# Optimization experiments

Measured on AMD Instinct MI355X. Metric: run time of the kernel, lower is better.

The kernel has to match this reference:

```python
import jax, jax.numpy as jnp
import numpy as np

B, L, K = 256, 128, 6
FA, FB, D = 39, 10, 128
R, T = 3, 2
NEG = -9e8


def _gru(x, h, wih, whh, bih, bhh):
    # torch.nn.GRUCell semantics
    gi = x @ wih.T + bih
    gh = h @ whh.T + bhh
    ir, iz, inn = jnp.split(gi, 3, axis=-1)
    hr, hz, hn = jnp.split(gh, 3, axis=-1)
    r = jax.nn.sigmoid(ir + hr)
    z = jax.nn.sigmoid(iz + hz)
    n = jnp.tanh(inn + r * hn)
    return (1.0 - z) * n + z * h


def _forward(atom_list, bond_list, atom_mask, atom_fc_w, atom_fc_b, nbr_fc_w, nbr_fc_b,
             align_w, align_b, attend_w, attend_b, gru_wih, gru_whh, gru_bih, gru_bhh,
             mol_align_w, mol_align_b, mol_attend_w, mol_attend_b,
             mol_gru_wih, mol_gru_whh, mol_gru_bih, mol_gru_bhh, out_w, out_b,
             atom_degree_list, bond_degree_list):
    lrelu = jax.nn.leaky_relu  # slope 0.01, matches torch default
    bidx = jnp.arange(atom_list.shape[0])[:, None, None]
    gather = lambda f, idx: f[bidx, idx]  # [B,L,F] gathered by [B,L,K] -> [B,L,K,F]

    atom_feature = lrelu(atom_list @ atom_fc_w + atom_fc_b)  # [B,L,D]
    nbr = jnp.concatenate([gather(atom_list, atom_degree_list),
                           gather(bond_list, bond_degree_list)], axis=-1)
    nbr = lrelu(nbr @ nbr_fc_w + nbr_fc_b)  # [B,L,K,D]

    pad = atom_list.shape[1] - 1  # mol_length-1 is padding sentinel
    attend_mask = (atom_degree_list != pad).astype(atom_feature.dtype)[..., None]
    softmax_mask = jnp.where(atom_degree_list == pad, NEG, 0.0).astype(atom_feature.dtype)[..., None]

    def attn(cur, nbr_feat, aw, ab, tw, tb):
        exp = jnp.broadcast_to(cur[:, :, None, :], nbr_feat.shape)
        score = lrelu(jnp.concatenate([exp, nbr_feat], axis=-1) @ aw + ab) + softmax_mask
        w = jax.nn.softmax(score, axis=-2) * attend_mask  # softmax over neighbors
        return jax.nn.elu(jnp.sum(w * (nbr_feat @ tw + tb), axis=-2))

    h = atom_feature
    ctx = attn(atom_feature, nbr, align_w[0], align_b[0], attend_w[0], attend_b[0])
    h = _gru(ctx, h, gru_wih[0], gru_whh[0], gru_bih[0], gru_bhh[0])
    act = jax.nn.relu(h)
    for d in range(1, R):
        nbr_f = gather(act, atom_degree_list)
        ctx = attn(act, nbr_f, align_w[d], align_b[d], attend_w[d], attend_b[d])
        h = _gru(ctx, h, gru_wih[d], gru_whh[d], gru_bih[d], gru_bhh[d])
        act = jax.nn.relu(h)

    am = atom_mask[..., None]  # [B,L,1]
    mol_feature = jnp.sum(act * am, axis=-2)  # [B,D]
    act_mol = jax.nn.relu(mol_feature)
    mol_smask = jnp.where(am == 0, NEG, 0.0).astype(atom_feature.dtype)
    for _ in range(T):
        exp = jnp.broadcast_to(act_mol[:, None, :], act.shape)
        score = lrelu(jnp.concatenate([exp, act], axis=-1) @ mol_align_w + mol_align_b) + mol_smask
        w = jax.nn.softmax(score, axis=-2) * am  # softmax over atoms
        ctx = jax.nn.elu(jnp.sum(w * (act @ mol_attend_w + mol_attend_b), axis=-2))
        mol_feature = _gru(ctx, mol_feature, mol_gru_wih, mol_gru_whh, mol_gru_bih, mol_gru_bhh)
        act_mol = jax.nn.relu(mol_feature)
    mol_prediction = mol_feature @ out_w + out_b  # [B,1]
    return h, mol_prediction


def setup_inputs():
    key = jax.random.key(0)
    ks = jax.random.split(key, 30)
    f = lambda i, s: jax.random.normal(ks[i], s, dtype=jnp.float32) * 0.1
    return {
        'atom_list': jax.random.normal(ks[0], (B, L, FA), dtype=jnp.float32),
        'bond_list': jax.random.normal(ks[1], (B, L, FB), dtype=jnp.float32),
        'atom_mask': jnp.ones((B, L), jnp.float32),
        'atom_fc_w': f(2, (FA, D)), 'atom_fc_b': f(3, (D,)),
        'nbr_fc_w': f(4, (FA + FB, D)), 'nbr_fc_b': f(5, (D,)),
        'align_w': f(6, (R, 2 * D, 1)), 'align_b': f(7, (R, 1)),
        'attend_w': f(8, (R, D, D)), 'attend_b': f(9, (R, D)),
        'gru_wih': f(10, (R, 3 * D, D)), 'gru_whh': f(11, (R, 3 * D, D)),
        'gru_bih': f(12, (R, 3 * D)), 'gru_bhh': f(13, (R, 3 * D)),
        'mol_align_w': f(14, (2 * D, 1)), 'mol_align_b': f(15, (1,)),
        'mol_attend_w': f(16, (D, D)), 'mol_attend_b': f(17, (D,)),
        'mol_gru_wih': f(18, (3 * D, D)), 'mol_gru_whh': f(19, (3 * D, D)),
        'mol_gru_bih': f(20, (3 * D,)), 'mol_gru_bhh': f(21, (3 * D,)),
        'out_w': f(22, (D, 1)), 'out_b': f(23, (1,)),
        'atom_degree_list': jax.random.randint(ks[24], (B, L, K), 0, L),
        'bond_degree_list': jax.random.randint(ks[25], (B, L, K), 0, L),
    }


def reference(atom_list, bond_list, atom_mask, atom_fc_w, atom_fc_b, nbr_fc_w, nbr_fc_b,
              align_w, align_b, attend_w, attend_b, gru_wih, gru_whh, gru_bih, gru_bhh,
              mol_align_w, mol_align_b, mol_attend_w, mol_attend_b,
              mol_gru_wih, mol_gru_whh, mol_gru_bih, mol_gru_bhh, out_w, out_b,
              atom_degree_list, bond_degree_list):
    return _forward(atom_list, bond_list, atom_mask, atom_fc_w, atom_fc_b, nbr_fc_w, nbr_fc_b,
                    align_w, align_b, attend_w, attend_b, gru_wih, gru_whh, gru_bih, gru_bhh,
                    mol_align_w, mol_align_b, mol_attend_w, mol_attend_b,
                    mol_gru_wih, mol_gru_whh, mol_gru_bih, mol_gru_bhh, out_w, out_b,
                    atom_degree_list, bond_degree_list)
```

## Files before the change

kernel.cpp:

```cpp
#include <hip/hip_runtime.h>
#include <cstddef>


#define B_ 256
#define L_ 128
#define K_ 6
#define FA_ 39
#define FB_ 10
#define D_ 128
#define PAD_ 127
#define NEGC (-9.0e8f)
#define NA 32
#define NPAIR (NA * K_)

typedef unsigned short u16;
typedef unsigned int u32;
using s8 = __attribute__((ext_vector_type(8))) short;
using f4 = __attribute__((ext_vector_type(4))) float;

#define WIH_H 0
#define WIH_L 49152
#define WHH_H 98304
#define WHH_L 147456
#define TW_H  196608
#define TW_L  212992
#define RND_BLK2 229376
#define NB16 (3 * RND_BLK2)
#define NMOLF (2 * 128 * 384)

__device__ __forceinline__ float lrelu(float x) { return x > 0.f ? x : 0.01f * x; }
__device__ __forceinline__ float eluf(float x)  { return x > 0.f ? x : expm1f(x); }
__device__ __forceinline__ float sigm(float x)  { return 1.f / (1.f + expf(-x)); }
__device__ __forceinline__ float b2f(u16 u) {
  union { u32 i; float f; } v; v.i = ((u32)u) << 16; return v.f;
}
__device__ __forceinline__ short f2b(float f) {
  union { float f; u32 i; } v; v.f = f;
  u32 x = v.i;
  return (short)(u16)((x + 0x7FFFu + ((x >> 16) & 1u)) >> 16);
}

__global__ __launch_bounds__(256) void k_tr(
    const float* __restrict__ gwih, const float* __restrict__ gwhh,
    const float* __restrict__ attw,
    const float* __restrict__ mwih, const float* __restrict__ mwhh,
    short* __restrict__ wB, float* __restrict__ molT) {
  int idx = blockIdx.x * 256 + threadIdx.x;
  if (idx < NB16) {
    int r = idx / RND_BLK2, o = idx % RND_BLK2;
    float v; int lo;
    int e, kind;
    if (o < 98304)      { kind = 0; lo = o / 49152; e = o % 49152; }
    else if (o < 196608){ kind = 1; int o2 = o - 98304; lo = o2 / 49152; e = o2 % 49152; }
    else                { kind = 2; int o2 = o - 196608; lo = o2 / 16384; e = o2 % 16384; }
    int gt = e >> 11, rem = e & 2047;
    int kc = rem >> 9, rem2 = rem & 511;
    int lane = rem2 >> 3, j = rem2 & 7;
    int col = lane & 15, quad = lane >> 4;
    int g = gt * 16 + col;
    int k = kc * 32 + quad * 8 + j;
    if (kind == 0)      v = gwih[(size_t)r * 49152 + g * 128 + k];
// ... 86 lines not shown
    const short* __restrict__ APg, float* __restrict__ Q0g)
{
  int tid = threadIdx.x;
  __shared__ float WbS[10 * 128];
  __shared__ float nbS[128], ahS[128];
  for (int i = tid; i < 10 * 128; i += 256)
    WbS[i] = nbr_w[(FA_ + i / 128) * D_ + (i % 128)];
  if (tid < 128) { nbS[tid] = nbr_b[tid]; ahS[tid] = aw0[D_ + tid]; }
  __syncthreads();

  int p = blockIdx.x * 64 + (tid >> 2);
  int seg = tid & 3;
  int aidx = adeg[p], bidx = bdeg[p];
  int bb = p / (L_ * K_);
  const short* rowA = APg + ((size_t)bb * L_ + aidx) * D_;
  const float* brow = bond_list + ((size_t)bb * L_ + bidx) * FB_;
  float bnd[10];
#pragma unroll
  for (int m = 0; m < 10; m++) bnd[m] = brow[m];
  float s = 0.f;
  int j0 = seg * 32;
#pragma unroll 4
  for (int j = j0; j < j0 + 32; j++) {
    float v = b2f((u16)rowA[j]) + nbS[j];
#pragma unroll
    for (int m = 0; m < 10; m++) v += bnd[m] * WbS[m * 128 + j];
    s += lrelu(v) * ahS[j];
  }
  s += __shfl_xor(s, 1, 64);
  s += __shfl_xor(s, 2, 64);
  if (seg == 0) Q0g[p] = s;
}

template <int FIRST>
__global__ __launch_bounds__(512, 4) void k_round(
    const u16* __restrict__ hin,
    u16* __restrict__ hout,
    const float* __restrict__ bond_list,
    const int* __restrict__ adeg, const int* __restrict__ bdeg,
    const float* __restrict__ nbr_w, const float* __restrict__ nbr_b,
    const short* __restrict__ APg,
    const float* __restrict__ ab,
    const float* __restrict__ awN,
    const float* __restrict__ tb,
    const short* __restrict__ wR,
    const float* __restrict__ bih, const float* __restrict__ bhh,
    const float* __restrict__ Pr, const float* __restrict__ Qr,
    float* __restrict__ Pw, float* __restrict__ Qw)
{
  int tid  = threadIdx.x;
  int lane = tid & 63;
  int wv   = tid >> 6;
  int quad = lane >> 4;
  int col  = lane & 15;
  int aT   = tid >> 4;
  int dg   = (tid & 15) * 8;
  int tile = (blockIdx.x & 7) * 128 + (blockIdx.x >> 3);
  int a0   = tile * NA;
  int bb   = a0 >> 7;

  const short* wihH = wR + WIH_H;
  const short* wihL = wR + WIH_L;
  const short* whhH = wR + WHH_H;
  const short* whhL = wR + WHH_L;
  const short* twH  = wR + TW_H;
  const short* twL  = wR + TW_L;

  __shared__ short hrowH[NA][136];
  __shared__ __align__(16) char arena[17408];
  __shared__ float awNS[256];
  __shared__ float partials[512];
  __shared__ float pS[NA], qS[NPAIR], wkS[NPAIR], wsS[NA];
  __shared__ int aidxS[NPAIR];
  __shared__ int bidxS[FIRST ? NPAIR : 1];
  __shared__ float bwS[FIRST ? 1920 : 1];

  short* ybarH = (short*)arena;
  short* ybarL = (short*)(arena + 8704);
  float* hnrel = (float*)arena;

  if (tid < NPAIR) {
    int av = adeg[a0 * K_ + tid];
    aidxS[tid] = av;
    if (FIRST) { bidxS[tid] = bdeg[a0 * K_ + tid]; qS[tid] = Qr[a0 * K_ + tid]; }
    else       qS[tid] = Qr[bb * L_ + av];
  } else if (tid < NPAIR + NA) {
    pS[tid - NPAIR] = Pr[a0 + (tid - NPAIR)];
  }
  if (tid < 256) awNS[tid] = awN[tid];
  __syncthreads();

  if (FIRST) {
    for (int i = tid; i < NPAIR * 10; i += 512) {
      int p = i / 10, m = i % 10;
      bwS[p * 10 + m] = bond_list[((size_t)bb * L_ + bidxS[p]) * FB_ + m];
    }
  }
  *(s8*)&hrowH[aT][dg] = *(const s8*)&hin[(size_t)(a0 + aT) * D_ + dg];

  if (tid < NA) {
    int a = tid;
    float abv = ab[0];
    float sc[K_];
    float m = -3.0e38f;
#pragma unroll
    for (int k = 0; k < K_; k++) {
      float s = lrelu(pS[a] + qS[a * K_ + k] + abv);
      if (aidxS[a * K_ + k] == PAD_) s += NEGC;
      sc[k] = s; m = fmaxf(m, s);
    }
    float es = 0.f;
#pragma unroll
    for (int k = 0; k < K_; k++) { sc[k] = expf(sc[k] - m); es += sc[k]; }
    float ws = 0.f;
#pragma unroll
    for (int k = 0; k < K_; k++) {
      float w = (aidxS[a * K_ + k] == PAD_) ? 0.f : sc[k] / es;
      wkS[a * K_ + k] = w; ws += w;
    }
    wsS[a] = ws;
  }
  __syncthreads();

  {
    float yb[8];
#pragma unroll
    for (int j = 0; j < 8; j++) yb[j] = 0.f;
    if (FIRST) {
#pragma unroll
      for (int h = 0; h < 2; h++) {
        float Wr[10][4];
#pragma unroll
        for (int m = 0; m < 10; m++) {
          float4 w = *(const float4*)&nbr_w[(FA_ + m) * D_ + dg + h * 4];
          Wr[m][0] = w.x; Wr[m][1] = w.y; Wr[m][2] = w.z; Wr[m][3] = w.w;
        }
        float4 nb4 = *(const float4*)&nbr_b[dg + h * 4];
        float nb[4] = {nb4.x, nb4.y, nb4.z, nb4.w};
#pragma unroll
        for (int k = 0; k < K_; k++) {
          int p = aT * K_ + k;
          ushort4 ap4 = *(const ushort4*)&APg[((size_t)bb * L_ + aidxS[p]) * D_ + dg + h * 4];
          float nf[4] = { b2f(ap4.x) + nb[0], b2f(ap4.y) + nb[1],
                          b2f(ap4.z) + nb[2], b2f(ap4.w) + nb[3] };
#pragma unroll
          for (int m = 0; m < 10; m++) {
            float bv = bwS[p * 10 + m];
#pragma unroll
            for (int j = 0; j < 4; j++) nf[j] += bv * Wr[m][j];
          }
          float w = wkS[p];
#pragma unroll
          for (int j = 0; j < 4; j++) yb[h * 4 + j] += w * lrelu(nf[j]);
        }
      }
    } else {
#pragma unroll
      for (int k = 0; k < K_; k++) {
        int p = aT * K_ + k;
        float w = wkS[p];
        s8 hv8 = *(const s8*)&hin[((size_t)bb * L_ + aidxS[p]) * D_ + dg];
#pragma unroll
        for (int j = 0; j < 8; j++) yb[j] += w * fmaxf(b2f((u16)hv8[j]), 0.f);
      }
    }
    s8 yh8, yl8;
#pragma unroll
    for (int j = 0; j < 8; j++) {
      short hi = f2b(yb[j]);
      yh8[j] = hi;
      yl8[j] = f2b(yb[j] - b2f((u16)hi));
    }
    *(s8*)&ybarH[aT * 136 + dg] = yh8;
    *(s8*)&ybarL[aT * 136 + dg] = yl8;
  }
  __syncthreads();

  {
    f4 c2[2] = {};
#pragma unroll
    for (int k0c = 0; k0c < 4; k0c++) {
      int fo = ((wv * 4 + k0c) * 64 + lane) * 8;
      s8 bwh = *(const s8*)&twH[fo];
      s8 bwl = *(const s8*)&twL[fo];
#pragma unroll
      for (int at = 0; at < 2; at++) {
        s8 ayh = *(const s8*)&ybarH[(at * 16 + col) * 136 + k0c * 32 + quad * 8];
        s8 ayl = *(const s8*)&ybarL[(at * 16 + col) * 136 + k0c * 32 + quad * 8];
        c2[at] = __builtin_amdgcn_mfma_f32_16x16x32_bf16(ayh, bwh, c2[at], 0, 0, 0);
        c2[at] = __builtin_amdgcn_mfma_f32_16x16x32_bf16(ayl, bwh, c2[at], 0, 0, 0);
        c2[at] = __builtin_amdgcn_mfma_f32_16x16x32_bf16(ayh, bwl, c2[at], 0, 0, 0);
      }
    }
    __syncthreads();
    int g = wv * 16 + col;
    float tbv = tb[g];
#pragma unroll
    for (int at = 0; at < 2; at++) {
#pragma unroll
      for (int r = 0; r < 4; r++) {
        int a = at * 16 + quad * 4 + r;
        float c = eluf(c2[at][r] + wsS[a] * tbv);
        short chs = f2b(c);
        ybarH[a * 136 + g] = chs;
        ybarL[a * 136 + g] = f2b(c - b2f((u16)chs));
      }
    }
  }
  __syncthreads();

  {
    const short* ctxH = ybarH;
    const short* ctxL = ybarL;
    f4 gi[2][3] = {}, gh[2][3] = {};
#pragma unroll
    for (int k0c = 0; k0c < 4; k0c++) {
      s8 ach[2], acl[2], ahh[2];
#pragma unroll
      for (int at = 0; at < 2; at++) {
        ach[at] = *(const s8*)&ctxH[(at * 16 + col) * 136 + k0c * 32 + quad * 8];
        acl[at] = *(const s8*)&ctxL[(at * 16 + col) * 136 + k0c * 32 + quad * 8];
        ahh[at] = *(const s8*)&hrowH[at * 16 + col][k0c * 32 + quad * 8];
      }
#pragma unroll
      for (int kd = 0; kd < 3; kd++) {
        int gt = wv + kd * 8;
        int fo = ((gt * 4 + k0c) * 64 + lane) * 8;
        s8 bi_h = *(const s8*)&wihH[fo];
        s8 bi_l = *(const s8*)&wihL[fo];
        s8 bh_h = *(const s8*)&whhH[fo];
        s8 bh_l = *(const s8*)&whhL[fo];
#pragma unroll
        for (int at = 0; at < 2; at++) {
          gi[at][kd] = __builtin_amdgcn_mfma_f32_16x16x32_bf16(ach[at], bi_h, gi[at][kd], 0, 0, 0);
          gi[at][kd] = __builtin_amdgcn_mfma_f32_16x16x32_bf16(acl[at], bi_h, gi[at][kd], 0, 0, 0);
          gi[at][kd] = __builtin_amdgcn_mfma_f32_16x16x32_bf16(ach[at], bi_l, gi[at][kd], 0, 0, 0);
          gh[at][kd] = __builtin_amdgcn_mfma_f32_16x16x32_bf16(ahh[at], bh_h, gh[at][kd], 0, 0, 0);
          gh[at][kd] = __builtin_amdgcn_mfma_f32_16x16x32_bf16(ahh[at], bh_l, gh[at][kd], 0, 0, 0);
        }
      }
    }
    __syncthreads();

    {
      int ic = wv * 16 + col;
      float bi0 = bih[ic], bi1 = bih[D_ + ic], bi2 = bih[2 * D_ + ic];
      float bh0 = bhh[ic], bh1 = bhh[D_ + ic], bh2 = bhh[2 * D_ + ic];
#pragma unroll
      for (int at = 0; at < 2; at++) {
#pragma unroll
        for (int r = 0; r < 4; r++) {
          int a = at * 16 + quad * 4 + r;
          float rr = sigm(gi[at][0][r] + bi0 + gh[at][0][r] + bh0);
          float zz = sigm(gi[at][1][r] + bi1 + gh[at][1][r] + bh1);
          float nn = tanhf(gi[at][2][r] + bi2 + rr * (gh[at][2][r] + bh2));
          float hv = b2f((u16)hrowH[a][ic]);
          float hn = (1.f - zz) * nn + zz * hv;
          hrowH[a][ic] = f2b(hn);
          if (Pw) hnrel[a * 132 + ic] = fmaxf(hn, 0.f);
        }
      }
    }
  }
  __syncthreads();

  *(s8*)&hout[(size_t)(a0 + aT) * D_ + dg] = *(const s8*)&hrowH[aT][dg];

  if (Pw) {
    {
      int a = tid >> 4, dt = (tid >> 3) & 1, seg = tid & 7;
      float s = 0.f;
#pragma unroll
      for (int j = 0; j < 16; j++)
        s += hnrel[a * 132 + seg * 16 + j] * awNS[dt * 128 + seg * 16 + j];
      partials[tid] = s;
    }
    __syncthreads();
    if (tid < 64) {
      int a = tid >> 1, dt = tid & 1;
      float s = 0.f;
#pragma unroll
      for (int seg = 0; seg < 8; seg++) s += partials[a * 16 + dt * 8 + seg];
      if (dt) Qw[a0 + a] = s; else Pw[a0 + a] = s;
    }
  }
}

__device__ __forceinline__ float blk_sum128(float v, int tid, float* redS) {
  if (tid < 128) {
#pragma unroll
    for (int s = 1; s < 64; s <<= 1) v += __shfl_xor(v, s, 64);
    if ((tid & 63) == 0) redS[tid >> 6] = v;
  }
  __syncthreads();
  float r = redS[0] + redS[1];
  __syncthreads();
  return r;
}
__device__ __forceinline__ float blk_max128(float v, int tid, float* redS) {
  if (tid < 128) {
#pragma unroll
    for (int s = 1; s < 64; s <<= 1) v = fmaxf(v, __shfl_xor(v, s, 64));
    if ((tid & 63) == 0) redS[tid >> 6] = v;
  }
  __syncthreads();
  float r = fmaxf(redS[0], redS[1]);
  __syncthreads();
  return r;
}

__global__ __launch_bounds__(512) void k_mol(
    const u16* __restrict__ hfin,
    float* __restrict__ hcopy,
    const float* __restrict__ amask,
    const float* __restrict__ maw, const float* __restrict__ mab,
    const float* __restrict__ mtw, const float* __restrict__ mtb,
    const float* __restrict__ wih_t, const float* __restrict__ whh_t,
    const float* __restrict__ bih, const float* __restrict__ bhh,
    const float* __restrict__ ow, const float* __restrict__ ob,
    float* __restrict__ pred)
{
  int b = blockIdx.x;
  int tid = threadIdx.x;
  int t128 = tid & 127;
  int qf = tid >> 7;
  __shared__ float actS[L_][D_ + 1];
  __shared__ float redS[2];
  __shared__ float par4[4][132];
  __shared__ float pg[3][6][132];
  __shared__ float wgt[128], ybv[132], ctx[132], mfS[132], amol[132];
  __shared__ float msk[128], mawh[128], scf[128];

  if (qf == 0) { msk[t128] = amask[b * L_ + t128]; mawh[t128] = maw[D_ + t128]; }
  for (int i = 0; i < 32; i++) {
    int l = qf * 32 + i;
    float hv = b2f(hfin[(size_t)(b * L_ + l) * D_ + t128]);
    hcopy[(size_t)(b * L_ + l) * D_ + t128] = hv;
    actS[l][t128] = fmaxf(hv, 0.f);
  }
  __syncthreads();

  {
    float s = 0.f;
    for (int i = 0; i < 32; i++) { int l = qf * 32 + i; s += actS[l][t128] * msk[l]; }
    par4[qf][t128] = s;
  }
  __syncthreads();
  if (qf == 0) {
    float mf = par4[0][t128] + par4[1][t128] + par4[2][t128] + par4[3][t128];
    mfS[t128] = mf; amol[t128] = fmaxf(mf, 0.f);
  }
  __syncthreads();

  float mabv = mab[0];

  for (int t = 0; t < 2; t++) {
    float s0 = blk_sum128((tid < 128) ? amol[tid] * maw[tid] : 0.f, tid, redS);

    {
      float s = 0.f;
      for (int i = 0; i < 32; i++) { int j = qf * 32 + i; s += actS[t128][j] * mawh[j]; }
      par4[qf][t128] = s;
    }
    __syncthreads();
    if (qf == 0) {
      float sc = lrelu(s0 + mabv + par4[0][t128] + par4[1][t128] + par4[2][t128] + par4[3][t128]);
      if (msk[t128] == 0.f) sc += NEGC;
      scf[t128] = sc;
    }
    __syncthreads();

    float scv = scf[t128];
    float mx = blk_max128((tid < 128) ? scv : -3.0e38f, tid, redS);
    float e = expf(scv - mx);
    float es = blk_sum128((tid < 128) ? e : 0.f, tid, redS);
    float w = (e / es) * msk[t128];
    if (qf == 0) wgt[t128] = w;
    float wsum = blk_sum128((tid < 128) ? w : 0.f, tid, redS);

    {
      float s = 0.f;
      for (int i = 0; i < 32; i++) { int l = qf * 32 + i; s += wgt[l] * actS[l][t128]; }
      par4[qf][t128] = s;
    }
    __syncthreads();
    if (qf == 0) ybv[t128] = par4[0][t128] + par4[1][t128] + par4[2][t128] + par4[3][t128];
    __syncthreads();

    {
      float s = 0.f;
#pragma unroll 2
      for (int i = 0; i < 32; i++) { int j = qf * 32 + i; s += ybv[j] * mtw[j * D_ + t128]; }
      par4[qf][t128] = s;
    }
    __syncthreads();
    if (qf == 0)
      ctx[t128] = eluf(par4[0][t128] + par4[1][t128] + par4[2][t128] + par4[3][t128]
                       + wsum * mtb[t128]);
    __syncthreads();

    {
      float gi0 = 0, gi1 = 0, gi2 = 0, gh0 = 0, gh1 = 0, gh2 = 0;
#pragma unroll 2
      for (int i = 0; i < 32; i++) {
        int j = qf * 32 + i;
        const float* wi = wih_t + (size_t)j * 384;
        const float* wh = whh_t + (size_t)j * 384;
        float xc = ctx[j], xh = mfS[j];
        gi0 += xc * wi[t128]; gi1 += xc * wi[128 + t128]; gi2 += xc * wi[256 + t128];
        gh0 += xh * wh[t128]; gh1 += xh * wh[128 + t128]; gh2 += xh * wh[256 + t128];
      }
      if (qf > 0) {
        pg[qf - 1][0][t128] = gi0; pg[qf - 1][1][t128] = gi1; pg[qf - 1][2][t128] = gi2;
        pg[qf - 1][3][t128] = gh0; pg[qf - 1][4][t128] = gh1; pg[qf - 1][5][t128] = gh2;
      }
      __syncthreads();
      if (qf == 0) {
        gi0 += pg[0][0][t128] + pg[1][0][t128] + pg[2][0][t128] + bih[t128];
        gi1 += pg[0][1][t128] + pg[1][1][t128] + pg[2][1][t128] + bih[128 + t128];
        gi2 += pg[0][2][t128] + pg[1][2][t128] + pg[2][2][t128] + bih[256 + t128];
        gh0 += pg[0][3][t128] + pg[1][3][t128] + pg[2][3][t128] + bhh[t128];
        gh1 += pg[0][4][t128] + pg[1][4][t128] + pg[2][4][t128] + bhh[128 + t128];
        gh2 += pg[0][5][t128] + pg[1][5][t128] + pg[2][5][t128] + bhh[256 + t128];
        float r = sigm(gi0 + gh0);
        float z = sigm(gi1 + gh1);
        float n = tanhf(gi2 + r * gh2);
        float hn = (1.f - z) * n + z * mfS[t128];
        mfS[t128] = hn;
        amol[t128] = fmaxf(hn, 0.f);
      }
      __syncthreads();
    }
  }

  float fin = blk_sum128((tid < 128) ? mfS[tid] * ow[tid] : 0.f, tid, redS);
  if (tid == 0) pred[b] = fin + ob[0];
}

extern "C" void kernel_launch(void* const* d_in, const int* in_sizes, int n_in,
                              void* d_out, int out_size, void* d_ws, size_t ws_size,
                              hipStream_t stream) {
  const float* atom_list    = (const float*)d_in[0];
  const float* bond_list    = (const float*)d_in[1];
  const float* atom_mask    = (const float*)d_in[2];
  const float* atom_fc_w    = (const float*)d_in[3];
  const float* atom_fc_b    = (const float*)d_in[4];
  const float* nbr_fc_w     = (const float*)d_in[5];
  const float* nbr_fc_b     = (const float*)d_in[6];
  const float* align_w      = (const float*)d_in[7];
  const float* align_b      = (const float*)d_in[8];
  const float* attend_w     = (const float*)d_in[9];
  const float* attend_b     = (const float*)d_in[10];
  const float* gru_wih      = (const float*)d_in[11];
  const float* gru_whh      = (const float*)d_in[12];
  const float* gru_bih      = (const float*)d_in[13];
  const float* gru_bhh      = (const float*)d_in[14];
  const float* mol_align_w  = (const float*)d_in[15];
  const float* mol_align_b  = (const float*)d_in[16];
  const float* mol_attend_w = (const float*)d_in[17];
  const float* mol_attend_b = (const float*)d_in[18];
  const float* mol_gru_wih  = (const float*)d_in[19];
  const float* mol_gru_whh  = (const float*)d_in[20];
  const float* mol_gru_bih  = (const float*)d_in[21];
  const float* mol_gru_bhh  = (const float*)d_in[22];
  const float* out_w        = (const float*)d_in[23];
  const float* out_b        = (const float*)d_in[24];
  const int*   adeg         = (const int*)d_in[25];
  const int*   bdeg         = (const int*)d_in[26];

  const size_t NH = (size_t)B_ * L_ * D_;
  u16*   hA   = (u16*)d_ws;
  u16*   hB   = hA + NH;
  short* wB   = (short*)(hB + NH);
  float* molT = (float*)(wB + NB16);
  float* PgA  = molT + NMOLF;
  float* QgA  = PgA + B_ * L_;
  float* PgB  = QgA + B_ * L_;
  float* QgB  = PgB + B_ * L_;
  short* APg  = (short*)(QgB + B_ * L_);
  float* Q0g  = (float*)(APg + NH);
  float* hOut = (float*)d_out;
  float* pred = hOut + NH;

  k_tr<<<dim3((NB16 + NMOLF + 255) / 256), dim3(256), 0, stream>>>(
      gru_wih, gru_whh, attend_w, mol_gru_wih, mol_gru_whh, wB, molT);

  k_pre<<<dim3(B_ * L_ / 16), dim3(128), 0, stream>>>(
      atom_list, atom_fc_w, atom_fc_b, nbr_fc_w, align_w, hA, APg, PgA);
  k_q0<<<dim3(B_ * L_ * K_ / 64), dim3(256), 0, stream>>>(
      bond_list, nbr_fc_w, nbr_fc_b, align_w, adeg, bdeg, APg, Q0g);

  dim3 blk(512), grd(B_ * L_ / NA);

  k_round<1><<<grd, blk, 0, stream>>>(
      hA, hB, bond_list, adeg, bdeg, nbr_fc_w, nbr_fc_b, APg,
      align_b, align_w + 2 * D_, attend_b,
      wB + 0 * (size_t)RND_BLK2, gru_bih, gru_bhh,
      PgA, Q0g, PgB, QgB);
  k_round<0><<<grd, blk, 0, stream>>>(
      hB, hA, bond_list, adeg, bdeg, nbr_fc_w, nbr_fc_b, APg,
      align_b + 1, align_w + 4 * D_, attend_b + D_,
      wB + 1 * (size_t)RND_BLK2, gru_bih + 3 * D_, gru_bhh + 3 * D_,
      PgB, QgB, PgA, QgA);
  k_round<0><<<grd, blk, 0, stream>>>(
      hA, hB, bond_list, adeg, bdeg, nbr_fc_w, nbr_fc_b, APg,
      align_b + 2, align_w + 4 * D_, attend_b + 2 * D_,
      wB + 2 * (size_t)RND_BLK2, gru_bih + 6 * D_, gru_bhh + 6 * D_,
      PgA, QgA, (float*)nullptr, (float*)nullptr);

  k_mol<<<dim3(B_), dim3(512), 0, stream>>>(
      hB, hOut, atom_mask, mol_align_w, mol_align_b, mol_attend_w, mol_attend_b,
      molT, molT + 128 * 384,
      mol_gru_bih, mol_gru_bhh, out_w, out_b, pred);
}
```

Baseline: 328.2 us.

## Fuse three message-passing rounds and molecule readout into one per-molecule kernel

Measured after the change: 808.5 us. +146.4%, slower.

```diff
diff --git a/kernel.cpp b/kernel.cpp
--- a/kernel.cpp
+++ b/kernel.cpp
@@ -10,8 +10,6 @@
 #define D_ 128
 #define PAD_ 127
 #define NEGC (-9.0e8f)
-#define NA 32
-#define NPAIR (NA * K_)
 
 typedef unsigned short u16;
 typedef unsigned int u32;
@@ -27,6 +25,20 @@
 #define RND_BLK2 229376
 #define NB16 (3 * RND_BLK2)
 #define NMOLF (2 * 128 * 384)
+
+#define OFF_HS     0
+#define OFF_ARENA  34816
+#define OFF_BWS    104448
+#define OFF_AIDX   135168
+#define OFF_WK     138240
+#define OFF_PA     141312
+#define OFF_QA     141824
+#define OFF_WS     142336
+#define OFF_AWN    142848
+#define OFF_PPART  143872
+#define OFF_QPART  147968
+#define OFF_MOLM   152064
+#define SMEM_BYTES 156176
 
 __device__ __forceinline__ float lrelu(float x) { return x > 0.f ? x : 0.01f * x; }
 __device__ __forceinline__ float eluf(float x)  { return x > 0.f ? x : expm1f(x); }
@@ -179,339 +191,359 @@
   if (seg == 0) Q0g[p] = s;
 }
 
-template <int FIRST>
-__global__ __launch_bounds__(512, 4) void k_round(
-    const u16* __restrict__ hin,
-    u16* __restrict__ hout,
+__device__ __forceinline__ float blk_sum128(float v, int tid, float* redS) {
+  if (tid < 128) {
+#pragma unroll
+    for (int s = 1; s < 64; s <<= 1) v += __shfl_xor(v, s, 64);
+    if ((tid & 63) == 0) redS[tid >> 6] = v;
+  }
+  __syncthreads();
+  float r = redS[0] + redS[1];
+  __syncthreads();
+  return r;
+}
+__device__ __forceinline__ float blk_max128(float v, int tid, float* redS) {
+  if (tid < 128) {
+#pragma unroll
+    for (int s = 1; s < 64; s <<= 1) v = fmaxf(v, __shfl_xor(v, s, 64));
+    if ((tid & 63) == 0) redS[tid >> 6] = v;
+  }
+  __syncthreads();
+  float r = fmaxf(redS[0], redS[1]);
+  __syncthreads();
+  return r;
+}
+
+__global__ __launch_bounds__(1024, 4) void k_mega(
+    const u16* __restrict__ hA,
     const float* __restrict__ bond_list,
     const int* __restrict__ adeg, const int* __restrict__ bdeg,
     const float* __restrict__ nbr_w, const float* __restrict__ nbr_b,
     const short* __restrict__ APg,
-    const float* __restrict__ ab,
-    const float* __restrict__ awN,
-    const float* __restrict__ tb,
-    const short* __restrict__ wR,
-    const float* __restrict__ bih, const float* __restrict__ bhh,
-    const float* __restrict__ Pr, const float* __restrict__ Qr,
-    float* __restrict__ Pw, float* __restrict__ Qw)
-{
-  int tid  = threadIdx.x;
-  int lane = tid & 63;
-  int wv   = tid >> 6;
-  int quad = lane >> 4;
-  int col  = lane & 15;
-  int aT   = tid >> 4;
-  int dg   = (tid & 15) * 8;
-  int tile = (blockIdx.x & 7) * 128 + (blockIdx.x >> 3);
-  int a0   = tile * NA;
-  int bb   = a0 >> 7;
-
-  const short* wihH = wR + WIH_H;
-  const short* wihL = wR + WIH_L;
-  const short* whhH = wR + WHH_H;
-  const short* whhL = wR + WHH_L;
-  const short* twH  = wR + TW_H;
-  const short* twL  = wR + TW_L;
-
-  __shared__ short hrowH[NA][136];
-  __shared__ __align__(16) char arena[17408];
-  __shared__ float awNS[256];
-  __shared__ float partials[512];
-  __shared__ float pS[NA], qS[NPAIR], wkS[NPAIR], wsS[NA];
-  __shared__ int aidxS[NPAIR];
-  __shared__ int bidxS[FIRST ? NPAIR : 1];
-  __shared__ float bwS[FIRST ? 1920 : 1];
-
-  short* ybarH = (short*)arena;
-  short* ybarL = (short*)(arena + 8704);
-  float* hnrel = (float*)arena;
-
-  if (tid < NPAIR) {
-    int av = adeg[a0 * K_ + tid];
-    aidxS[tid] = av;
-    if (FIRST) { bidxS[tid] = bdeg[a0 * K_ + tid]; qS[tid] = Qr[a0 * K_ + tid]; }
-    else       qS[tid] = Qr[bb * L_ + av];
-  } else if (tid < NPAIR + NA) {
-    pS[tid - NPAIR] = Pr[a0 + (tid - NPAIR)];
-  }
-  if (tid < 256) awNS[tid] = awN[tid];
-  __syncthreads();
-
-  if (FIRST) {
-    for (int i = tid; i < NPAIR * 10; i += 512) {
-      int p = i / 10, m = i % 10;
-      bwS[p * 10 + m] = bond_list[((size_t)bb * L_ + bidxS[p]) * FB_ + m];
-    }
-  }
-  *(s8*)&hrowH[aT][dg] = *(const s8*)&hin[(size_t)(a0 + aT) * D_ + dg];
-
-  if (tid < NA) {
-    int a = tid;
-    float abv = ab[0];
-    float sc[K_];
-    float m = -3.0e38f;
-#pragma unroll
-    for (int k = 0; k < K_; k++) {
-      float s = lrelu(pS[a] + qS[a * K_ + k] + abv);
-      if (aidxS[a * K_ + k] == PAD_) s += NEGC;
-      sc[k] = s; m = fmaxf(m, s);
-    }
-    float es = 0.f;
-#pragma unroll
-    for (int k = 0; k < K_; k++) { sc[k] = expf(sc[k] - m); es += sc[k]; }
-    float ws = 0.f;
-#pragma unroll
-    for (int k = 0; k < K_; k++) {
-      float w = (aidxS[a * K_ + k] == PAD_) ? 0.f : sc[k] / es;
-      wkS[a * K_ + k] = w; ws += w;
-    }
-    wsS[a] = ws;
-  }
-  __syncthreads();
-
-  {
-    float yb[8];
-#pragma unroll
-    for (int j = 0; j < 8; j++) yb[j] = 0.f;
-    if (FIRST) {
-#pragma unroll
-      for (int h = 0; h < 2; h++) {
-        float Wr[10][4];
-#pragma unroll
-        for (int m = 0; m < 10; m++) {
-          float4 w = *(const float4*)&nbr_w[(FA_ + m) * D_ + dg + h * 4];
-          Wr[m][0] = w.x; Wr[m][1] = w.y; Wr[m][2] = w.z; Wr[m][3] = w.w;
-        }
-        float4 nb4 = *(const float4*)&nbr_b[dg + h * 4];
-        float nb[4] = {nb4.x, nb4.y, nb4.z, nb4.w};
-#pragma unroll
-        for (int k = 0; k < K_; k++) {
-          int p = aT * K_ + k;
-          ushort4 ap4 = *(const ushort4*)&APg[((size_t)bb * L_ + aidxS[p]) * D_ + dg + h * 4];
-          float nf[4] = { b2f(ap4.x) + nb[0], b2f(ap4.y) + nb[1],
-                          b2f(ap4.z) + nb[2], b2f(ap4.w) + nb[3] };
-#pragma unroll
-          for (int m = 0; m < 10; m++) {
-            float bv = bwS[p * 10 + m];
-#pragma unroll
-            for (int j = 0; j < 4; j++) nf[j] += bv * Wr[m][j];
-          }
-          float w = wkS[p];
-#pragma unroll
-          for (int j = 0; j < 4; j++) yb[h * 4 + j] += w * lrelu(nf[j]);
-        }
-      }
-    } else {
-#pragma unroll
-      for (int k = 0; k < K_; k++) {
-        int p = aT * K_ + k;
-        float w = wkS[p];
-        s8 hv8 = *(const s8*)&hin[((size_t)bb * L_ + aidxS[p]) * D_ + dg];
-#pragma unroll
-        for (int j = 0; j < 8; j++) yb[j] += w * fmaxf(b2f((u16)hv8[j]), 0.f);
-      }
-    }
-    s8 yh8, yl8;
-#pragma unroll
-    for (int j = 0; j < 8; j++) {
-      short hi = f2b(yb[j]);
-      yh8[j] = hi;
-      yl8[j] = f2b(yb[j] - b2f((u16)hi));
-    }
-    *(s8*)&ybarH[aT * 136 + dg] = yh8;
-    *(s8*)&ybarL[aT * 136 + dg] = yl8;
-  }
-  __syncthreads();
-
-  {
-    f4 c2[2] = {};
-#pragma unroll
-    for (int k0c = 0; k0c < 4; k0c++) {
-      int fo = ((wv * 4 + k0c) * 64 + lane) * 8;
-      s8 bwh = *(const s8*)&twH[fo];
-      s8 bwl = *(const s8*)&twL[fo];
-#pragma unroll
-      for (int at = 0; at < 2; at++) {
-        s8 ayh = *(const s8*)&ybarH[(at * 16 + col) * 136 + k0c * 32 + quad * 8];
-        s8 ayl = *(const s8*)&ybarL[(at * 16 + col) * 136 + k0c * 32 + quad * 8];
-        c2[at] = __builtin_amdgcn_mfma_f32_16x16x32_bf16(ayh, bwh, c2[at], 0, 0, 0);
-        c2[at] = __builtin_amdgcn_mfma_f32_16x16x32_bf16(ayl, bwh, c2[at], 0, 0, 0);
-        c2[at] = __builtin_amdgcn_mfma_f32_16x16x32_bf16(ayh, bwl, c2[at], 0, 0, 0);
-      }
-    }
-    __syncthreads();
-    int g = wv * 16 + col;
-    float tbv = tb[g];
-#pragma unroll
-    for (int at = 0; at < 2; at++) {
-#pragma unroll
-      for (int r = 0; r < 4; r++) {
-        int a = at * 16 + quad * 4 + r;
-        float c = eluf(c2[at][r] + wsS[a] * tbv);
-        short chs = f2b(c);
-        ybarH[a * 136 + g] = chs;
-        ybarL[a * 136 + g] = f2b(c - b2f((u16)chs));
-      }
-    }
-  }
-  __syncthreads();
-
-  {
-    const short* ctxH = ybarH;
-    const short* ctxL = ybarL;
-    f4 gi[2][3] = {}, gh[2][3] = {};
-#pragma unroll
-    for (int k0c = 0; k0c < 4; k0c++) {
-      s8 ach[2], acl[2], ahh[2];
-#pragma unroll
-      for (int at = 0; at < 2; at++) {
-        ach[at] = *(const s8*)&ctxH[(at * 16 + col) * 136 + k0c * 32 + quad * 8];
-        acl[at] = *(const s8*)&ctxL[(at * 16 + col) * 136 + k0c * 32 + quad * 8];
-        ahh[at] = *(const s8*)&hrowH[at * 16 + col][k0c * 32 + quad * 8];
-      }
-#pragma unroll
-      for (int kd = 0; kd < 3; kd++) {
-        int gt = wv + kd * 8;
-        int fo = ((gt * 4 + k0c) * 64 + lane) * 8;
-        s8 bi_h = *(const s8*)&wihH[fo];
-        s8 bi_l = *(const s8*)&wihL[fo];
-        s8 bh_h = *(const s8*)&whhH[fo];
-        s8 bh_l = *(const s8*)&whhL[fo];
-#pragma unroll
-        for (int at = 0; at < 2; at++) {
-          gi[at][kd] = __builtin_amdgcn_mfma_f32_16x16x32_bf16(ach[at], bi_h, gi[at][kd], 0, 0, 0);
-          gi[at][kd] = __builtin_amdgcn_mfma_f32_16x16x32_bf16(acl[at], bi_h, gi[at][kd], 0, 0, 0);
-          gi[at][kd] = __builtin_amdgcn_mfma_f32_16x16x32_bf16(ach[at], bi_l, gi[at][kd], 0, 0, 0);
-          gh[at][kd] = __builtin_amdgcn_mfma_f32_16x16x32_bf16(ahh[at], bh_h, gh[at][kd], 0, 0, 0);
-          gh[at][kd] = __builtin_amdgcn_mfma_f32_16x16x32_bf16(ahh[at], bh_l, gh[at][kd], 0, 0, 0);
-        }
-      }
-    }
-    __syncthreads();
-
-    {
-      int ic = wv * 16 + col;
-      float bi0 = bih[ic], bi1 = bih[D_ + ic], bi2 = bih[2 * D_ + ic];
-      float bh0 = bhh[ic], bh1 = bhh[D_ + ic], bh2 = bhh[2 * D_ + ic];
-#pragma unroll
-      for (int at = 0; at < 2; at++) {
-#pragma unroll
-        for (int r = 0; r < 4; r++) {
-          int a = at * 16 + quad * 4 + r;
-          float rr = sigm(gi[at][0][r] + bi0 + gh[at][0][r] + bh0);
-          float zz = sigm(gi[at][1][r] + bi1 + gh[at][1][r] + bh1);
-          float nn = tanhf(gi[at][2][r] + bi2 + rr * (gh[at][2][r] + bh2));
-          float hv = b2f((u16)hrowH[a][ic]);
-          float hn = (1.f - zz) * nn + zz * hv;
-          hrowH[a][ic] = f2b(hn);
-          if (Pw) hnrel[a * 132 + ic] = fmaxf(hn, 0.f);
-        }
-      }
-    }
-  }
-  __syncthreads();
-
-  *(s8*)&hout[(size_t)(a0 + aT) * D_ + dg] = *(const s8*)&hrowH[aT][dg];
-
-  if (Pw) {
-    {
-      int a = tid >> 4, dt = (tid >> 3) & 1, seg = tid & 7;
-      float s = 0.f;
-#pragma unroll
-      for (int j = 0; j < 16; j++)
-        s += hnrel[a * 132 + seg * 16 + j] * awNS[dt * 128 + seg * 16 + j];
-      partials[tid] = s;
-    }
-    __syncthreads();
-    if (tid < 64) {
-      int a = tid >> 1, dt = tid & 1;
-      float s = 0.f;
-#pragma unroll
-      for (int seg = 0; seg < 8; seg++) s += partials[a * 16 + dt * 8 + seg];
-      if (dt) Qw[a0 + a] = s; else Pw[a0 + a] = s;
-    }
-  }
-}
-
-__device__ __forceinline__ float blk_sum128(float v, int tid, float* redS) {
-  if (tid < 128) {
-#pragma unroll
-    for (int s = 1; s < 64; s <<= 1) v += __shfl_xor(v, s, 64);
-    if ((tid & 63) == 0) redS[tid >> 6] = v;
-  }
-  __syncthreads();
-  float r = redS[0] + redS[1];
-  __syncthreads();
-  return r;
-}
-__device__ __forceinline__ float blk_max128(float v, int tid, float* redS) {
-  if (tid < 128) {
-#pragma unroll
-    for (int s = 1; s < 64; s <<= 1) v = fmaxf(v, __shfl_xor(v, s, 64));
-    if ((tid & 63) == 0) redS[tid >> 6] = v;
-  }
-  __syncthreads();
-  float r = fmaxf(redS[0], redS[1]);
-  __syncthreads();
-  return r;
-}
-
-__global__ __launch_bounds__(512) void k_mol(
-    const u16* __restrict__ hfin,
-    float* __restrict__ hcopy,
+    const float* __restrict__ align_b_all,
+    const float* __restrict__ align_w_all,
+    const float* __restrict__ attend_b_all,
+    const short* __restrict__ wB,
+    const float* __restrict__ bih_all, const float* __restrict__ bhh_all,
+    const float* __restrict__ PgA, const float* __restrict__ Q0g,
     const float* __restrict__ amask,
     const float* __restrict__ maw, const float* __restrict__ mab,
     const float* __restrict__ mtw, const float* __restrict__ mtb,
     const float* __restrict__ wih_t, const float* __restrict__ whh_t,
-    const float* __restrict__ bih, const float* __restrict__ bhh,
+    const float* __restrict__ mbih, const float* __restrict__ mbhh,
     const float* __restrict__ ow, const float* __restrict__ ob,
-    float* __restrict__ pred)
+    float* __restrict__ hcopy, float* __restrict__ pred)
 {
-  int b = blockIdx.x;
-  int tid = threadIdx.x;
+  __shared__ __align__(16) char smem[SMEM_BYTES];
+  short* hS    = (short*)(smem + OFF_HS);
+  char*  arena = smem + OFF_ARENA;
+  short* ybH   = (short*)arena;
+  short* ybL   = (short*)(arena + 34816);
+  float* actS  = (float*)arena;
+  float* bwS   = (float*)(smem + OFF_BWS);
+  float* pg    = bwS;
+  float* par8  = bwS + 5544;
+  int*   aidxS = (int*)(smem + OFF_AIDX);
+  float* wkS   = (float*)(smem + OFF_WK);
+  float* pAS   = (float*)(smem + OFF_PA);
+  float* qAS   = (float*)(smem + OFF_QA);
+  float* wsS   = (float*)(smem + OFF_WS);
+  float* awNS  = (float*)(smem + OFF_AWN);
+  float* pPart = (float*)(smem + OFF_PPART);
+  float* qPart = (float*)(smem + OFF_QPART);
+  float* molm  = (float*)(smem + OFF_MOLM);
+  float* wgt = molm, *ybv = molm + 128, *ctxv = molm + 256, *mfS = molm + 384,
+       *amol = molm + 512, *msk = molm + 640, *mawh = molm + 768,
+       *scf = molm + 896, *redS = molm + 1024;
+
+  int tid  = threadIdx.x;
+  int lane = tid & 63;
+  int wv   = tid >> 6;
+  int wl   = wv & 7;
+  int wg   = wv >> 3;
+  int quad = lane >> 4;
+  int col  = lane & 15;
+  int bb   = blockIdx.x;
+
+  if (tid < 768) aidxS[tid] = adeg[bb * 768 + tid];
+  if (tid < 128) pAS[tid] = PgA[bb * 128 + tid];
+  {
+    int l = tid >> 3, c = (tid & 7) * 16;
+    *(s8*)&hS[l * 136 + c]     = *(const s8*)&hA[((size_t)bb * 128 + l) * 128 + c];
+    *(s8*)&hS[l * 136 + c + 8] = *(const s8*)&hA[((size_t)bb * 128 + l) * 128 + c + 8];
+  }
+  for (int i = tid; i < 7680; i += 1024) {
+    int p = i / 10, m = i % 10;
+    bwS[i] = bond_list[((size_t)bb * 128 + bdeg[bb * 768 + p]) * 10 + m];
+  }
+
+  for (int r = 0; r < 3; r++) {
+    const short* wihH = wB + (size_t)r * RND_BLK2 + WIH_H;
+    const short* wihL = wB + (size_t)r * RND_BLK2 + WIH_L;
+    const short* whhH = wB + (size_t)r * RND_BLK2 + WHH_H;
+    const short* whhL = wB + (size_t)r * RND_BLK2 + WHH_L;
+    const short* twH  = wB + (size_t)r * RND_BLK2 + TW_H;
+    const short* twL  = wB + (size_t)r * RND_BLK2 + TW_L;
+    const float* bihr = bih_all + 3 * D_ * r;
+    const float* bhhr = bhh_all + 3 * D_ * r;
+
+    __syncthreads();
+
+    if (tid < 128) {
+      int a = tid;
+      float abv = align_b_all[r];
+      float sc[K_];
+      float m = -3.0e38f;
+#pragma unroll
+      for (int k = 0; k < K_; k++) {
+        int av = aidxS[a * K_ + k];
+        float qv = (r == 0) ? Q0g[bb * 768 + a * K_ + k] : qAS[av];
+        float s = lrelu(pAS[a] + qv + abv);
+        if (av == PAD_) s += NEGC;
+        sc[k] = s; m = fmaxf(m, s);
+      }
+      float es = 0.f;
+#pragma unroll
+      for (int k = 0; k < K_; k++) { sc[k] = expf(sc[k] - m); es += sc[k]; }
+      float ws = 0.f;
+#pragma unroll
+      for (int k = 0; k < K_; k++) {
+        float w = (aidxS[a * K_ + k] == PAD_) ? 0.f : sc[k] / es;
+        wkS[a * K_ + k] = w; ws += w;
+      }
+      wsS[a] = ws;
+    } else if (tid >= 512 && tid < 768 && r < 2) {
+      awNS[tid - 512] = align_w_all[(r + 1) * 2 * D_ + (tid - 512)];
+    }
+    __syncthreads();
+
+    {
+      int aT  = tid >> 3;
+      int dgq = (tid & 7) * 16;
+      float yb[16];
+#pragma unroll
+      for (int j = 0; j < 16; j++) yb[j] = 0.f;
+      if (r == 0) {
+#pragma unroll
+        for (int c = 0; c < 4; c++) {
+          int d0 = dgq + c * 4;
+          float wr[10][4];
+#pragma unroll
+          for (int m = 0; m < 10; m++) {
+            float4 w = *(const float4*)&nbr_w[(FA_ + m) * D_ + d0];
+            wr[m][0] = w.x; wr[m][1] = w.y; wr[m][2] = w.z; wr[m][3] = w.w;
+          }
+          float4 nb4 = *(const float4*)&nbr_b[d0];
+          float nb[4] = {nb4.x, nb4.y, nb4.z, nb4.w};
+#pragma unroll
+          for (int k = 0; k < K_; k++) {
+            int p = aT * K_ + k;
+            ushort4 ap4 = *(const ushort4*)&APg[((size_t)bb * 128 + aidxS[p]) * 128 + d0];
+            float nf[4] = { b2f(ap4.x) + nb[0], b2f(ap4.y) + nb[1],
+                            b2f(ap4.z) + nb[2], b2f(ap4.w) + nb[3] };
+#pragma unroll
+            for (int m = 0; m < 10; m++) {
+              float bv = bwS[p * 10 + m];
+#pragma unroll
+              for (int j = 0; j < 4; j++) nf[j] += bv * wr[m][j];
+            }
+            float w = wkS[p];
+#pragma unroll
+            for (int j = 0; j < 4; j++) yb[c * 4 + j] += w * lrelu(nf[j]);
+          }
+        }
+      } else {
+#pragma unroll
+        for (int k = 0; k < K_; k++) {
+          int p = aT * K_ + k;
+          float w = wkS[p];
+          int av = aidxS[p];
+          s8 h0 = *(const s8*)&hS[av * 136 + dgq];
+          s8 h1 = *(const s8*)&hS[av * 136 + dgq + 8];
+#pragma unroll
+          for (int j = 0; j < 8; j++) {
+            yb[j]     += w * fmaxf(b2f((u16)h0[j]), 0.f);
+            yb[8 + j] += w * fmaxf(b2f((u16)h1[j]), 0.f);
+          }
+        }
+      }
+      s8 yh0, yl0, yh1, yl1;
+#pragma unroll
+      for (int j = 0; j < 8; j++) {
+        short hi0 = f2b(yb[j]);
+        yh0[j] = hi0; yl0[j] = f2b(yb[j] - b2f((u16)hi0));
+        short hi1 = f2b(yb[8 + j]);
+        yh1[j] = hi1; yl1[j] = f2b(yb[8 + j] - b2f((u16)hi1));
+      }
+      *(s8*)&ybH[aT * 136 + dgq]     = yh0;
+      *(s8*)&ybL[aT * 136 + dgq]     = yl0;
+      *(s8*)&ybH[aT * 136 + dgq + 8] = yh1;
+      *(s8*)&ybL[aT * 136 + dgq + 8] = yl1;
+    }
+    __syncthreads();
+
+    {
+      f4 c2[2][2] = {};
+#pragma unroll
+      for (int k0c = 0; k0c < 4; k0c++) {
+        int fo = ((wl * 4 + k0c) * 64 + lane) * 8;
+        s8 bwh = *(const s8*)&twH[fo];
+        s8 bwl_ = *(const s8*)&twL[fo];
+#pragma unroll
+        for (int p = 0; p < 2; p++)
+#pragma unroll
+          for (int at = 0; at < 2; at++) {
+            int row = p * 64 + wg * 32 + at * 16 + col;
+            s8 ayh = *(const s8*)&ybH[row * 136 + k0c * 32 + quad * 8];
+            s8 ayl = *(const s8*)&ybL[row * 136 + k0c * 32 + quad * 8];
+            c2[p][at] = __builtin_amdgcn_mfma_f32_16x16x32_bf16(ayh, bwh, c2[p][at], 0, 0, 0);
+            c2[p][at] = __builtin_amdgcn_mfma_f32_16x16x32_bf16(ayl, bwh, c2[p][at], 0, 0, 0);
+            c2[p][at] = __builtin_amdgcn_mfma_f32_16x16x32_bf16(ayh, bwl_, c2[p][at], 0, 0, 0);
+          }
+      }
+      __syncthreads();
+      int g = wl * 16 + col;
+      float tbv = attend_b_all[r * D_ + g];
+#pragma unroll
+      for (int p = 0; p < 2; p++)
+#pragma unroll
+        for (int at = 0; at < 2; at++)
+#pragma unroll
+          for (int rr = 0; rr < 4; rr++) {
+            int a = p * 64 + wg * 32 + at * 16 + quad * 4 + rr;
+            float cx = eluf(c2[p][at][rr] + wsS[a] * tbv);
+            short chs = f2b(cx);
+            ybH[a * 136 + g] = chs;
+            ybL[a * 136 + g] = f2b(cx - b2f((u16)chs));
+          }
+    }
+    __syncthreads();
+
+    {
+      int ic = wl * 16 + col;
+      float bi0 = bihr[ic], bi1 = bihr[D_ + ic], bi2 = bihr[2 * D_ + ic];
+      float bh0 = bhhr[ic], bh1 = bhhr[D_ + ic], bh2 = bhhr[2 * D_ + ic];
+#pragma unroll 1
+      for (int p = 0; p < 2; p++) {
+        f4 gi[2][3] = {}, gh[2][3] = {};
+#pragma unroll
+        for (int k0c = 0; k0c < 4; k0c++) {
+          s8 ach[2], acl[2], ahh[2];
+#pragma unroll
+          for (int at = 0; at < 2; at++) {
+            int row = p * 64 + wg * 32 + at * 16 + col;
+            ach[at] = *(const s8*)&ybH[row * 136 + k0c * 32 + quad * 8];
+            acl[at] = *(const s8*)&ybL[row * 136 + k0c * 32 + quad * 8];
+            ahh[at] = *(const s8*)&hS[row * 136 + k0c * 32 + quad * 8];
+          }
+#pragma unroll
+          for (int kd = 0; kd < 3; kd++) {
+            int gt = wl + kd * 8;
+            int fo = ((gt * 4 + k0c) * 64 + lane) * 8;
+            s8 bi_h = *(const s8*)&wihH[fo];
+            s8 bi_l = *(const s8*)&wihL[fo];
+            s8 bh_h = *(const s8*)&whhH[fo];
+            s8 bh_l = *(const s8*)&whhL[fo];
+#pragma unroll
+            for (int at = 0; at < 2; at++) {
+              gi[at][kd] = __builtin_amdgcn_mfma_f32_16x16x32_bf16(ach[at], bi_h, gi[at][kd], 0, 0, 0);
+              gi[at][kd] = __builtin_amdgcn_mfma_f32_16x16x32_bf16(acl[at], bi_h, gi[at][kd], 0, 0, 0);
+              gi[at][kd] = __builtin_amdgcn_mfma_f32_16x16x32_bf16(ach[at], bi_l, gi[at][kd], 0, 0, 0);
+              gh[at][kd] = __builtin_amdgcn_mfma_f32_16x16x32_bf16(ahh[at], bh_h, gh[at][kd], 0, 0, 0);
+              gh[at][kd] = __builtin_amdgcn_mfma_f32_16x16x32_bf16(ahh[at], bh_l, gh[at][kd], 0, 0, 0);
+            }
+          }
+        }
+        __syncthreads();
+#pragma unroll
+        for (int at = 0; at < 2; at++)
+#pragma unroll
+          for (int rr = 0; rr < 4; rr++) {
+            int a = p * 64 + wg * 32 + at * 16 + quad * 4 + rr;
+            float r_ = sigm(gi[at][0][rr] + bi0 + gh[at][0][rr] + bh0);
+            float z_ = sigm(gi[at][1][rr] + bi1 + gh[at][1][rr] + bh1);
+            float n_ = tanhf(gi[at][2][rr] + bi2 + r_ * (gh[at][2][rr] + bh2));
+            float hv = b2f((u16)hS[a * 136 + ic]);
+            float hn = (1.f - z_) * n_ + z_ * hv;
+            hS[a * 136 + ic] = f2b(hn);
+            if (r < 2) {
+              float hr = fmaxf(hn, 0.f);
+              float vp = hr * awNS[ic];
+              float vq = hr * awNS[128 + ic];
+              vp += __shfl_xor(vp, 1, 64); vp += __shfl_xor(vp, 2, 64);
+              vp += __shfl_xor(vp, 4, 64); vp += __shfl_xor(vp, 8, 64);
+              vq += __shfl_xor(vq, 1, 64); vq += __shfl_xor(vq, 2, 64);
+              vq += __shfl_xor(vq, 4, 64); vq += __shfl_xor(vq, 8, 64);
+              if (col == 0) { pPart[wl * 128 + a] = vp; qPart[wl * 128 + a] = vq; }
+            }
+          }
+      }
+    }
+    __syncthreads();
+
+    if (r < 2 && tid < 256) {
+      int a = tid & 127;
+      const float* src = (tid < 128) ? pPart : qPart;
+      float s = 0.f;
+#pragma unroll
+      for (int w = 0; w < 8; w++) s += src[w * 128 + a];
+      if (tid < 128) pAS[a] = s; else qAS[a] = s;
+    }
+  }
+  __syncthreads();
+
   int t128 = tid & 127;
-  int qf = tid >> 7;
-  __shared__ float actS[L_][D_ + 1];
-  __shared__ float redS[2];
-  __shared__ float par4[4][132];
-  __shared__ float pg[3][6][132];
-  __shared__ float wgt[128], ybv[132], ctx[132], mfS[132], amol[132];
-  __shared__ float msk[128], mawh[128], scf[128];
-
-  if (qf == 0) { msk[t128] = amask[b * L_ + t128]; mawh[t128] = maw[D_ + t128]; }
-  for (int i = 0; i < 32; i++) {
-    int l = qf * 32 + i;
-    float hv = b2f(hfin[(size_t)(b * L_ + l) * D_ + t128]);
-    hcopy[(size_t)(b * L_ + l) * D_ + t128] = hv;
-    actS[l][t128] = fmaxf(hv, 0.f);
-  }
+  int ef   = tid >> 7;
+  {
+    int l = tid >> 3, c = (tid & 7) * 16;
+#pragma unroll
+    for (int hh = 0; hh < 2; hh++) {
+      s8 h8 = *(const s8*)&hS[l * 136 + c + hh * 8];
+      float hv[8];
+#pragma unroll
+      for (int j = 0; j < 8; j++) hv[j] = b2f((u16)h8[j]);
+      float4 o0 = {hv[0], hv[1], hv[2], hv[3]};
+      float4 o1 = {hv[4], hv[5], hv[6], hv[7]};
+      *(float4*)&hcopy[((size_t)bb * 128 + l) * 128 + c + hh * 8] = o0;
+      *(float4*)&hcopy[((size_t)bb * 128 + l) * 128 + c + hh * 8 + 4] = o1;
+#pragma unroll
+      for (int j = 0; j < 8; j++) actS[l * 129 + c + hh * 8 + j] = fmaxf(hv[j], 0.f);
+    }
+  }
+  if (tid < 128) { msk[tid] = amask[bb * 128 + tid]; mawh[tid] = maw[D_ + tid]; }
   __syncthreads();
 
   {
     float s = 0.f;
-    for (int i = 0; i < 32; i++) { int l = qf * 32 + i; s += actS[l][t128] * msk[l]; }
-    par4[qf][t128] = s;
-  }
-  __syncthreads();
-  if (qf == 0) {
-    float mf = par4[0][t128] + par4[1][t128] + par4[2][t128] + par4[3][t128];
+#pragma unroll 2
+    for (int i = 0; i < 16; i++) { int l = ef * 16 + i; s += actS[l * 129 + t128] * msk[l]; }
+    par8[ef * 132 + t128] = s;
+  }
+  __syncthreads();
+  if (ef == 0) {
+    float mf = 0.f;
+#pragma unroll
+    for (int e = 0; e < 8; e++) mf += par8[e * 132 + t128];
     mfS[t128] = mf; amol[t128] = fmaxf(mf, 0.f);
   }
   __syncthreads();
 
   float mabv = mab[0];
-
   for (int t = 0; t < 2; t++) {
     float s0 = blk_sum128((tid < 128) ? amol[tid] * maw[tid] : 0.f, tid, redS);
 
     {
       float s = 0.f;
-      for (int i = 0; i < 32; i++) { int j = qf * 32 + i; s += actS[t128][j] * mawh[j]; }
-      par4[qf][t128] = s;
-    }
-    __syncthreads();
-    if (qf == 0) {
-      float sc = lrelu(s0 + mabv + par4[0][t128] + par4[1][t128] + par4[2][t128] + par4[3][t128]);
+#pragma unroll 2
+      for (int i = 0; i < 16; i++) { int j = ef * 16 + i; s += actS[t128 * 129 + j] * mawh[j]; }
+      par8[ef * 132 + t128] = s;
+    }
+    __syncthreads();
+    if (ef == 0) {
+      float sc = s0 + mabv;
+#pragma unroll
+      for (int e = 0; e < 8; e++) sc += par8[e * 132 + t128];
+      sc = lrelu(sc);
       if (msk[t128] == 0.f) sc += NEGC;
       scf[t128] = sc;
     }
@@ -522,57 +554,75 @@
     float e = expf(scv - mx);
     float es = blk_sum128((tid < 128) ? e : 0.f, tid, redS);
     float w = (e / es) * msk[t128];
-    if (qf == 0) wgt[t128] = w;
+    if (tid < 128) wgt[t128] = w;
     float wsum = blk_sum128((tid < 128) ? w : 0.f, tid, redS);
-
-    {
-      float s = 0.f;
-      for (int i = 0; i < 32; i++) { int l = qf * 32 + i; s += wgt[l] * actS[l][t128]; }
-      par4[qf][t128] = s;
-    }
-    __syncthreads();
-    if (qf == 0) ybv[t128] = par4[0][t128] + par4[1][t128] + par4[2][t128] + par4[3][t128];
-    __syncthreads();
 
     {
       float s = 0.f;
 #pragma unroll 2
-      for (int i = 0; i < 32; i++) { int j = qf * 32 + i; s += ybv[j] * mtw[j * D_ + t128]; }
-      par4[qf][t128] = s;
-    }
-    __syncthreads();
-    if (qf == 0)
-      ctx[t128] = eluf(par4[0][t128] + par4[1][t128] + par4[2][t128] + par4[3][t128]
-                       + wsum * mtb[t128]);
+      for (int i = 0; i < 16; i++) { int l = ef * 16 + i; s += wgt[l] * actS[l * 129 + t128]; }
+      par8[ef * 132 + t128] = s;
+    }
+    __syncthreads();
+    if (ef == 0) {
+      float y = 0.f;
+#pragma unroll
+      for (int e2 = 0; e2 < 8; e2++) y += par8[e2 * 132 + t128];
+      ybv[t128] = y;
+    }
+    __syncthreads();
+
+    {
+      float s = 0.f;
+#pragma unroll 2
+      for (int i = 0; i < 16; i++) { int j = ef * 16 + i; s += ybv[j] * mtw[j * D_ + t128]; }
+      par8[ef * 132 + t128] = s;
+    }
+    __syncthreads();
+    if (ef == 0) {
+      float cx = wsum * mtb[t128];
+#pragma unroll
+      for (int e2 = 0; e2 < 8; e2++) cx += par8[e2 * 132 + t128];
+      ctxv[t128] = eluf(cx);
+    }
     __syncthreads();
 
     {
       float gi0 = 0, gi1 = 0, gi2 = 0, gh0 = 0, gh1 = 0, gh2 = 0;
 #pragma unroll 2
-      for (int i = 0; i < 32; i++) {
-        int j = qf * 32 + i;
+      for (int i = 0; i < 16; i++) {
+        int j = ef * 16 + i;
         const float* wi = wih_t + (size_t)j * 384;
         const float* wh = whh_t + (size_t)j * 384;
-        float xc = ctx[j], xh = mfS[j];
+        float xc = ctxv[j], xh = mfS[j];
         gi0 += xc * wi[t128]; gi1 += xc * wi[128 + t128]; gi2 += xc * wi[256 + t128];
         gh0 += xh * wh[t128]; gh1 += xh * wh[128 + t128]; gh2 += xh * wh[256 + t128];
       }
-      if (qf > 0) {
-        pg[qf - 1][0][t128] = gi0; pg[qf - 1][1][t128] = gi1; pg[qf - 1][2][t128] = gi2;
-        pg[qf - 1][3][t128] = gh0; pg[qf - 1][4][t128] = gh1; pg[qf - 1][5][t128] = gh2;
+      if (ef > 0) {
+        pg[((ef - 1) * 6 + 0) * 132 + t128] = gi0;
+        pg[((ef - 1) * 6 + 1) * 132 + t128] = gi1;
+        pg[((ef - 1) * 6 + 2) * 132 + t128] = gi2;
+        pg[((ef - 1) * 6 + 3) * 132 + t128] = gh0;
+        pg[((ef - 1) * 6 + 4) * 132 + t128] = gh1;
+        pg[((ef - 1) * 6 + 5) * 132 + t128] = gh2;
       }
       __syncthreads();
-      if (qf == 0) {
-        gi0 += pg[0][0][t128] + pg[1][0][t128] + pg[2][0][t128] + bih[t128];
-        gi1 += pg[0][1][t128] + pg[1][1][t128] + pg[2][1][t128] + bih[128 + t128];
-        gi2 += pg[0][2][t128] + pg[1][2][t128] + pg[2][2][t128] + bih[256 + t128];
-        gh0 += pg[0][3][t128] + pg[1][3][t128] + pg[2][3][t128] + bhh[t128];
-        gh1 += pg[0][4][t128] + pg[1][4][t128] + pg[2][4][t128] + bhh[128 + t128];
-        gh2 += pg[0][5][t128] + pg[1][5][t128] + pg[2][5][t128] + bhh[256 + t128];
-        float r = sigm(gi0 + gh0);
-        float z = sigm(gi1 + gh1);
-        float n = tanhf(gi2 + r * gh2);
-        float hn = (1.f - z) * n + z * mfS[t128];
+      if (ef == 0) {
+#pragma unroll
+        for (int e2 = 0; e2 < 7; e2++) {
+          gi0 += pg[(e2 * 6 + 0) * 132 + t128];
+          gi1 += pg[(e2 * 6 + 1) * 132 + t128];
+          gi2 += pg[(e2 * 6 + 2) * 132 + t128];
+          gh0 += pg[(e2 * 6 + 3) * 132 + t128];
+          gh1 += pg[(e2 * 6 + 4) * 132 + t128];
+          gh2 += pg[(e2 * 6 + 5) * 132 + t128];
+        }
+        gi0 += mbih[t128]; gi1 += mbih[128 + t128]; gi2 += mbih[256 + t128];
+        gh0 += mbhh[t128]; gh1 += mbhh[128 + t128]; gh2 += mbhh[256 + t128];
+        float r_ = sigm(gi0 + gh0);
+        float z_ = sigm(gi1 + gh1);
+        float n_ = tanhf(gi2 + r_ * gh2);
+        float hn = (1.f - z_) * n_ + z_ * mfS[t128];
         mfS[t128] = hn;
         amol[t128] = fmaxf(hn, 0.f);
       }
@@ -581,7 +631,7 @@
   }
 
   float fin = blk_sum128((tid < 128) ? mfS[tid] * ow[tid] : 0.f, tid, redS);
-  if (tid == 0) pred[b] = fin + ob[0];
+  if (tid == 0) pred[bb] = fin + ob[0];
 }
 
 extern "C" void kernel_launch(void* const* d_in, const int* in_sizes, int n_in,
@@ -637,26 +687,11 @@
   k_q0<<<dim3(B_ * L_ * K_ / 64), dim3(256), 0, stream>>>(
       bond_list, nbr_fc_w, nbr_fc_b, align_w, adeg, bdeg, APg, Q0g);
 
-  dim3 blk(512), grd(B_ * L_ / NA);
-
-  k_round<1><<<grd, blk, 0, stream>>>(
-      hA, hB, bond_list, adeg, bdeg, nbr_fc_w, nbr_fc_b, APg,
-      align_b, align_w + 2 * D_, attend_b,
-      wB + 0 * (size_t)RND_BLK2, gru_bih, gru_bhh,
-      PgA, Q0g, PgB, QgB);
-  k_round<0><<<grd, blk, 0, stream>>>(
-      hB, hA, bond_list, adeg, bdeg, nbr_fc_w, nbr_fc_b, APg,
-      align_b + 1, align_w + 4 * D_, attend_b + D_,
-      wB + 1 * (size_t)RND_BLK2, gru_bih + 3 * D_, gru_bhh + 3 * D_,
-      PgB, QgB, PgA, QgA);
-  k_round<0><<<grd, blk, 0, stream>>>(
-      hA, hB, bond_list, adeg, bdeg, nbr_fc_w, nbr_fc_b, APg,
-      align_b + 2, align_w + 4 * D_, attend_b + 2 * D_,
-      wB + 2 * (size_t)RND_BLK2, gru_bih + 6 * D_, gru_bhh + 6 * D_,
-      PgA, QgA, (float*)nullptr, (float*)nullptr);
-
-  k_mol<<<dim3(B_), dim3(512), 0, stream>>>(
-      hB, hOut, atom_mask, mol_align_w, mol_align_b, mol_attend_w, mol_attend_b,
-      molT, molT + 128 * 384,
-      mol_gru_bih, mol_gru_bhh, out_w, out_b, pred);
-}
+  k_mega<<<dim3(B_), dim3(1024), 0, stream>>>(
+      hA, bond_list, adeg, bdeg, nbr_fc_w, nbr_fc_b, APg,
+      align_b, align_w, attend_b, wB, gru_bih, gru_bhh,
+      PgA, Q0g,
+      atom_mask, mol_align_w, mol_align_b, mol_attend_w, mol_attend_b,
+      molT, molT + 128 * 384, mol_gru_bih, mol_gru_bhh, out_w, out_b,
+      hOut, pred);
+}
```
